# Kernel optimization log

Measured on AMD Instinct MI355X. Metric: run time of the kernel, lower is better.

Reference implementation:

```python
import jax, jax.numpy as jnp
import numpy as np


def setup_inputs() -> dict:
    key = jax.random.key(0)
    k1, k2 = jax.random.split(key)
    B, C = 32768, 1000
    output = jax.random.normal(k1, (B, C), dtype=jnp.float32)
    target = jax.random.randint(k2, (B,), 0, C, dtype=jnp.int64)
    return {"output": output, "target": target}


def _soft_hinge_loss(margin, output, target):
    B = output.shape[0]
    rows = jnp.arange(B)
    fst = jax.nn.relu(1.0 - margin)
    # relu(1 - z_y + logsumexp(z))
    snd = jax.nn.relu(1.0 - output[rows, target]
                      + jax.scipy.special.logsumexp(output, axis=1))
    return jnp.where(margin >= 0, fst, snd)


def _partial_opt_mask(loss_value, threshold):
    # Vectorized form of the serial cumulative-threshold loop:
    # sort ascending, accumulate L over ALL sorted values, select sorted
    # position idx iff cumsum <= threshold - idx.
    B = loss_value.shape[0]
    order = jnp.argsort(loss_value)
    sorted_loss = loss_value[order]
    cum = jnp.cumsum(sorted_loss)
    selected = cum <= (threshold - jnp.arange(B, dtype=loss_value.dtype))
    # scatter selection flags back to original sample positions -> 0/1 vector v
    v = jnp.zeros((B,), dtype=loss_value.dtype).at[order].set(
        selected.astype(loss_value.dtype))
    return v


def reference(output, target):
    B = output.shape[0]
    rows = jnp.arange(B)
    prob = jax.nn.softmax(output, axis=1)                 # [B, C]
    margin = prob[rows, target] - jnp.max(prob, axis=1)   # [B]
    l = _soft_hinge_loss(margin, output, target)          # [B]
    threshold = jnp.asarray(B, dtype=l.dtype)
    v = _partial_opt_mask(l, threshold)                   # [B] 0/1 mask
    curriculum_loss_1 = jnp.dot(v, l)
    curriculum_loss_2 = (jnp.asarray(B, l.dtype) - jnp.sum(v)
                         + jnp.sum((margin < 0).astype(l.dtype)))
    return jnp.where(curriculum_loss_1 < curriculum_loss_2,
                     curriculum_loss_2, curriculum_loss_1)
```

## Files before the change

kernel.cpp:

```cpp
#include <hip/hip_runtime.h>
#include <math.h>

#define WAVE 64
#define NBINS 8192
#define BIN_SHIFT 19

__device__ __forceinline__ float wave_incl_scan(float x) {
  const int lane = threadIdx.x & 63;
#pragma unroll
  for (int o = 1; o < 64; o <<= 1) {
    float t = __shfl_up(x, o, WAVE);
    if (lane >= o) x += t;
  }
  return x;
}

__global__ void row_loss_kernel(const float* __restrict__ outp,
                                const int* __restrict__ target,
                                float* __restrict__ lv,
                                int B, int C) {
  const int lane = threadIdx.x & (WAVE - 1);
  const int wid  = threadIdx.x >> 6;
  const int row  = blockIdx.x * (blockDim.x >> 6) + wid;
  if (row >= B) return;

  const float* rp = outp + (size_t)row * (size_t)C;
  const float zy = rp[target[row]];

  const int C4 = C >> 2;
  const float4* rp4 = (const float4*)rp;

  float m = -INFINITY, s = 0.f;
#pragma unroll 2
  for (int i = lane; i < C4; i += WAVE) {
    float4 v = rp4[i];
    m = fmaxf(fmaxf(m, fmaxf(v.x, v.y)), fmaxf(v.z, v.w));
    s += __expf(v.x) + __expf(v.y) + __expf(v.z) + __expf(v.w);
  }
  for (int i = (C4 << 2) + lane; i < C; i += WAVE) {
    float x = rp[i];
    m = fmaxf(m, x);
    s += __expf(x);
  }
#pragma unroll
  for (int o = 32; o; o >>= 1) {
    m = fmaxf(m, __shfl_xor(m, o, WAVE));
    s += __shfl_xor(s, o, WAVE);
  }

  if (lane == 0) {
    float l = (zy >= m) ? 1.0f : fmaxf(0.0f, 1.0f - zy + __logf(s));
    lv[row] = l;
  }
}

__global__ __launch_bounds__(1024)
void hist_kernel(const float* __restrict__ lv,
                 unsigned* __restrict__ hcnt,
                 float* __restrict__ hsum,
                 unsigned* __restrict__ n_one,
                 int B) {
  __shared__ unsigned scnt[NBINS];
  __shared__ float    ssum[NBINS];
  __shared__ unsigned s_one;

  const int tid = threadIdx.x;
  for (int i = tid; i < NBINS; i += 1024) { scnt[i] = 0u; ssum[i] = 0.f; }
  if (tid == 0) s_one = 0u;
  __syncthreads();

  const int gid = blockIdx.x * 1024 + tid;
  if (gid < B) {
    float v = lv[gid];
    unsigned bits = __float_as_uint(v);
    unsigned b = bits >> BIN_SHIFT;
    atomicAdd(&scnt[b], 1u);
    atomicAdd(&ssum[b], v);
    unsigned long long ball = __ballot(bits == 0x3F800000u);
    if ((tid & 63) == 0 && ball)
      atomicAdd(&s_one, (unsigned)__popcll(ball));
  }
  __syncthreads();

  for (int i = tid; i < NBINS; i += 1024) {
    unsigned c = scnt[i];
    if (c) {
      atomicAdd(&hcnt[i], c);
      atomicAdd(&hsum[i], ssum[i]);
    }
  }
  if (tid == 0 && s_one) atomicAdd(n_one, s_one);
}

__global__ __launch_bounds__(1024)
void scan_hist(const unsigned* __restrict__ hcnt,
               const float* __restrict__ hsum,
               const unsigned* __restrict__ n_one_p,
               float* __restrict__ out, int B) {
  const int tid = threadIdx.x;
  const int lane = tid & 63, wid = tid >> 6;
  __shared__ float wS[16], wC[16];
  __shared__ unsigned sh_first;

  const int BPT = NBINS / 1024;
  float bs[8], bn[8];
  float ls = 0.f, lc = 0.f;
#pragma unroll
  for (int i = 0; i < 8; i++) {
    int b = tid * BPT + i;
    bs[i] = hsum[b];
    bn[i] = (float)hcnt[b];
    ls += bs[i]; lc += bn[i];
  }

  const float cn = (float)B - (float)(*n_one_p);
  if (tid == 0) sh_first = 0xFFFFFFFFu;

  float is = wave_incl_scan(ls);
  float ic = wave_incl_scan(lc);
  if (lane == 63) { wS[wid] = is; wC[wid] = ic; }
  __syncthreads();
  if (wid == 0 && lane < 16) {
    float x = wS[lane], y = wC[lane];
    float xs = x, ys = y;
#pragma unroll
    for (int o = 1; o < 16; o <<= 1) {
      float t = __shfl_up(xs, o, WAVE);
      float u = __shfl_up(ys, o, WAVE);
      if (lane >= o) { xs += t; ys += u; }
    }
    wS[lane] = xs - x;
    wC[lane] = ys - y;
  }
  __syncthreads();

  float cS = wS[wid] + (is - ls);
  float cC = wC[wid] + (ic - lc);
  int fidx = -1; float fS = 0.f, fC = 0.f;
#pragma unroll
  for (int i = 0; i < 8; i++) {
    if (fidx < 0 && (cS + bs[i]) + (cC + bn[i]) - 1.f > (float)B) {
      fidx = i; fS = cS; fC = cC;
    }
    cS += bs[i]; cC += bn[i];
  }
  if (fidx >= 0) atomicMin(&sh_first, (unsigned)tid);
  __syncthreads();

  const double Bd = (double)B;
  if (sh_first == (unsigned)tid && fidx >= 0) {
    const unsigned bin = (unsigned)(tid * BPT + fidx);
    const double v  = (double)__uint_as_float(bin << BIN_SHIFT);
    const double S0 = (double)fS, K0 = (double)fC;
    const double mt = (double)bn[fidx];
    double j = floor((Bd - S0 - K0 + 1.0) / (v + 1.0));
    if (j < 0.0) j = 0.0;
    if (j > mt) j = mt;
    double loss1 = S0 + j * v;
    double loss2 = Bd - (K0 + j) + (double)cn;
    out[0] = (float)fmax(loss1, loss2);
  } else if (sh_first == 0xFFFFFFFFu && tid == 1023) {
    double loss1 = (double)cS;
    double loss2 = (double)cn;
    out[0] = (float)fmax(loss1, loss2);
  }
}

extern "C" void kernel_launch(void* const* d_in, const int* in_sizes, int n_in,
                              void* d_out, int out_size, void* d_ws, size_t ws_size,
                              hipStream_t stream) {
  const float* outp  = (const float*)d_in[0];
  const int* target  = (const int*)d_in[1];
  const int B = in_sizes[1];
  const int C = in_sizes[0] / B;

  float*    lv   = (float*)d_ws;
  unsigned* hcnt = (unsigned*)((char*)d_ws + (size_t)B * 4);
  float*    hsum = (float*)((char*)d_ws + (size_t)B * 4 + NBINS * 4);
  unsigned* none = (unsigned*)((char*)d_ws + (size_t)B * 4 + NBINS * 8);

  hipMemsetAsync((char*)d_ws + (size_t)B * 4, 0, NBINS * 8 + 16, stream);

  const int waves_per_block = 4;
  dim3 grid((B + waves_per_block - 1) / waves_per_block);
  row_loss_kernel<<<grid, waves_per_block * WAVE, 0, stream>>>(outp, target, lv, B, C);

  const int hblocks = (B + 1023) / 1024;
  hist_kernel<<<hblocks, 1024, 0, stream>>>(lv, hcnt, hsum, none, B);
  scan_hist<<<1, 1024, 0, stream>>>(hcnt, hsum, none, (float*)d_out, B);
}
```

Before: 39.49 us.

## Spread each row across four waves with one float4 per thread

The row loss kernel now assigns 256 threads (four waves) to each row and packs two rows per 512-thread block. Each thread loads a single float4 and computes its partial max and sum-exp. The per-wave partials are combined through shared memory, and one thread then computes the loss. The aim is more memory requests in flight and less serial looping per wave on a bandwidth-bound pass. The trade-off is a block-level barrier, and the kernel silently assumes C/4 <= 256, so wider rows would be computed wrong. The histogram kernel also swaps its ballot-based count of losses equal to 1.0 for a shuffle reduction, and the scan kernel gets cosmetic cleanups.

```diff
diff --git a/kernel.cpp b/kernel.cpp
--- a/kernel.cpp
+++ b/kernel.cpp
@@ -15,41 +15,50 @@
   return x;
 }
 
-__global__ void row_loss_kernel(const float* __restrict__ outp,
-                                const int* __restrict__ target,
-                                float* __restrict__ lv,
-                                int B, int C) {
-  const int lane = threadIdx.x & (WAVE - 1);
-  const int wid  = threadIdx.x >> 6;
-  const int row  = blockIdx.x * (blockDim.x >> 6) + wid;
-  if (row >= B) return;
-
-  const float* rp = outp + (size_t)row * (size_t)C;
-  const float zy = rp[target[row]];
-
+__global__ __launch_bounds__(512)
+void row_loss_kernel(const float* __restrict__ outp,
+                     const int* __restrict__ target,
+                     float* __restrict__ lv,
+                     int B, int C) {
+  const int sub  = threadIdx.x >> 8;
+  const int t    = threadIdx.x & 255;
+  const int lane = threadIdx.x & 63;
+  const int wsub = (threadIdx.x >> 6) & 3;
+  const int row  = blockIdx.x * 2 + sub;
+  const bool valid = (row < B);
+
+  __shared__ float pm[2][4], ps[2][4];
+
+  const float* rp = outp + (size_t)(valid ? row : 0) * (size_t)C;
   const int C4 = C >> 2;
-  const float4* rp4 = (const float4*)rp;
 
   float m = -INFINITY, s = 0.f;
-#pragma unroll 2
-  for (int i = lane; i < C4; i += WAVE) {
-    float4 v = rp4[i];
-    m = fmaxf(fmaxf(m, fmaxf(v.x, v.y)), fmaxf(v.z, v.w));
-    s += __expf(v.x) + __expf(v.y) + __expf(v.z) + __expf(v.w);
-  }
-  for (int i = (C4 << 2) + lane; i < C; i += WAVE) {
-    float x = rp[i];
-    m = fmaxf(m, x);
-    s += __expf(x);
+  if (valid && t < C4) {
+    const float4 v = ((const float4*)rp)[t];
+    m = fmaxf(fmaxf(v.x, v.y), fmaxf(v.z, v.w));
+    s = __expf(v.x) + __expf(v.y) + __expf(v.z) + __expf(v.w);
+  }
+  if (valid) {
+    for (int i = (C4 << 2) + t; i < C; i += 256) {
+      const float x = rp[i];
+      m = fmaxf(m, x);
+      s += __expf(x);
+    }
   }
 #pragma unroll
   for (int o = 32; o; o >>= 1) {
     m = fmaxf(m, __shfl_xor(m, o, WAVE));
     s += __shfl_xor(s, o, WAVE);
   }
-
-  if (lane == 0) {
-    float l = (zy >= m) ? 1.0f : fmaxf(0.0f, 1.0f - zy + __logf(s));
+  if (lane == 0) { pm[sub][wsub] = m; ps[sub][wsub] = s; }
+  __syncthreads();
+
+  if (valid && wsub == 0 && lane == 0) {
+    const float M = fmaxf(fmaxf(pm[sub][0], pm[sub][1]),
+                          fmaxf(pm[sub][2], pm[sub][3]));
+    const float S = ps[sub][0] + ps[sub][1] + ps[sub][2] + ps[sub][3];
+    const float zy = rp[target[row]];
+    const float l = (zy >= M) ? 1.0f : fmaxf(0.0f, 1.0f - zy + __logf(S));
     lv[row] = l;
   }
 }
@@ -65,25 +74,30 @@
   __shared__ unsigned s_one;
 
   const int tid = threadIdx.x;
+  const int lane = tid & 63;
+
   for (int i = tid; i < NBINS; i += 1024) { scnt[i] = 0u; ssum[i] = 0.f; }
   if (tid == 0) s_one = 0u;
   __syncthreads();
 
   const int gid = blockIdx.x * 1024 + tid;
+  int ones = 0;
   if (gid < B) {
-    float v = lv[gid];
-    unsigned bits = __float_as_uint(v);
-    unsigned b = bits >> BIN_SHIFT;
+    const float v = lv[gid];
+    const unsigned bits = __float_as_uint(v);
+    if (bits == 0x3F800000u) ones++;
+    const unsigned b = bits >> BIN_SHIFT;
     atomicAdd(&scnt[b], 1u);
     atomicAdd(&ssum[b], v);
-    unsigned long long ball = __ballot(bits == 0x3F800000u);
-    if ((tid & 63) == 0 && ball)
-      atomicAdd(&s_one, (unsigned)__popcll(ball));
-  }
+  }
+  float of = (float)ones;
+#pragma unroll
+  for (int o = 32; o; o >>= 1) of += __shfl_xor(of, o, WAVE);
+  if (lane == 0 && of > 0.f) atomicAdd(&s_one, (unsigned)of);
   __syncthreads();
 
   for (int i = tid; i < NBINS; i += 1024) {
-    unsigned c = scnt[i];
+    const unsigned c = scnt[i];
     if (c) {
       atomicAdd(&hcnt[i], c);
       atomicAdd(&hsum[i], ssum[i]);
@@ -102,14 +116,13 @@
   __shared__ float wS[16], wC[16];
   __shared__ unsigned sh_first;
 
-  const int BPT = NBINS / 1024;
   float bs[8], bn[8];
   float ls = 0.f, lc = 0.f;
+  const int b0 = tid * 8;
 #pragma unroll
   for (int i = 0; i < 8; i++) {
-    int b = tid * BPT + i;
-    bs[i] = hsum[b];
-    bn[i] = (float)hcnt[b];
+    bs[i] = hsum[b0 + i];
+    bn[i] = (float)hcnt[b0 + i];
     ls += bs[i]; lc += bn[i];
   }
 
@@ -125,9 +138,9 @@
     float xs = x, ys = y;
 #pragma unroll
     for (int o = 1; o < 16; o <<= 1) {
-      float t = __shfl_up(xs, o, WAVE);
-      float u = __shfl_up(ys, o, WAVE);
-      if (lane >= o) { xs += t; ys += u; }
+      float a = __shfl_up(xs, o, WAVE);
+      float b = __shfl_up(ys, o, WAVE);
+      if (lane >= o) { xs += a; ys += b; }
     }
     wS[lane] = xs - x;
     wC[lane] = ys - y;
@@ -149,19 +162,19 @@
 
   const double Bd = (double)B;
   if (sh_first == (unsigned)tid && fidx >= 0) {
-    const unsigned bin = (unsigned)(tid * BPT + fidx);
+    const unsigned bin = (unsigned)(tid * 8 + fidx);
     const double v  = (double)__uint_as_float(bin << BIN_SHIFT);
     const double S0 = (double)fS, K0 = (double)fC;
     const double mt = (double)bn[fidx];
     double j = floor((Bd - S0 - K0 + 1.0) / (v + 1.0));
     if (j < 0.0) j = 0.0;
     if (j > mt) j = mt;
-    double loss1 = S0 + j * v;
-    double loss2 = Bd - (K0 + j) + (double)cn;
+    const double loss1 = S0 + j * v;
+    const double loss2 = Bd - (K0 + j) + (double)cn;
     out[0] = (float)fmax(loss1, loss2);
   } else if (sh_first == 0xFFFFFFFFu && tid == 1023) {
-    double loss1 = (double)cS;
-    double loss2 = (double)cn;
+    const double loss1 = (double)cS;
+    const double loss2 = (double)cn;
     out[0] = (float)fmax(loss1, loss2);
   }
 }
@@ -181,9 +194,8 @@
 
   hipMemsetAsync((char*)d_ws + (size_t)B * 4, 0, NBINS * 8 + 16, stream);
 
-  const int waves_per_block = 4;
-  dim3 grid((B + waves_per_block - 1) / waves_per_block);
-  row_loss_kernel<<<grid, waves_per_block * WAVE, 0, stream>>>(outp, target, lv, B, C);
+  dim3 grid((B + 1) / 2);
+  row_loss_kernel<<<grid, 512, 0, stream>>>(outp, target, lv, B, C);
 
   const int hblocks = (B + 1023) / 1024;
   hist_kernel<<<hblocks, 1024, 0, stream>>>(lv, hcnt, hsum, none, B);
```

Measured after the change: 46.11 us. +16.8%, slower.
